# Kernel tuning notes

Measured on AMD Instinct MI355X. Metric: run time of the kernel, lower is better.

## Reference

```python
import jax, jax.numpy as jnp
import numpy as np

D = 1024

def setup_inputs() -> dict:
    key = jax.random.key(0)
    kx, kw = jax.random.split(key)
    x = jax.random.normal(kx, (4, 2048, D), dtype=jnp.float32)
    # nn.Linear(d, 3d, bias=False): weight [3d, d]; y = x @ W.T
    W = jax.random.normal(kw, (3 * D, D), dtype=jnp.float32) * (1.0 / np.sqrt(D))
    return {"x": x, "W": W}

def reference(x, W):
    d = x.shape[-1]
    qkv = jnp.einsum('bsd,ed->bse', x, W)  # [B,S,3d]
    q, k, v = jnp.split(qkv, 3, axis=2)
    att = jnp.einsum('bqd,bkd->bqk', q, k) * (1.0 / jnp.sqrt(jnp.asarray(d, x.dtype)))
    att = jax.nn.softmax(att, axis=-1)
    y = jnp.einsum('bqk,bkd->bqd', att, v)
    return y
```

## Files before the change

### kernel.cpp

```cpp
#include <hip/hip_runtime.h>
#include <hip/hip_bf16.h>

typedef __attribute__((ext_vector_type(8))) short short8;
typedef __attribute__((ext_vector_type(4))) float f32x4;

typedef unsigned short u16;

__device__ __forceinline__ u16 f32_to_bf16(float f) {
    unsigned int u = __float_as_uint(f);
    u += 0x7fffu + ((u >> 16) & 1u);
    return (u16)(u >> 16);
}
__device__ __forceinline__ float bf16_to_f32(u16 h) {
    return __uint_as_float(((unsigned int)h) << 16);
}

__device__ __forceinline__ void gload16(const u16* g, u16* lds_base) {
    __builtin_amdgcn_global_load_lds(
        (const __attribute__((address_space(1))) void*)g,
        (__attribute__((address_space(3))) void*)lds_base, 16, 0, 0);
}

__global__ void cast_inputs(const float* __restrict__ x, u16* __restrict__ Xb,
                            const float* __restrict__ W, u16* __restrict__ Wb,
                            int nx4, int nw4) {
    int i = blockIdx.x * blockDim.x + threadIdx.x;
    const float* in; u16* out; int idx;
    if (i < nx4) { in = x; out = Xb; idx = i; }
    else { idx = i - nx4; if (idx >= nw4) return; in = W; out = Wb; }
    float4 v = ((const float4*)in)[idx];
    ushort4 o;
    o.x = f32_to_bf16(v.x); o.y = f32_to_bf16(v.y);
    o.z = f32_to_bf16(v.z); o.w = f32_to_bf16(v.w);
    ((ushort4*)out)[idx] = o;
}


struct Frag128 { f32x4 acc[4][4]; int lane, wm, wn; };

__device__ __forceinline__ void gemm_core_128(
    const u16* __restrict__ A, const u16* __restrict__ Bt, int K, int lda, int ldb,
    int row0, int col0, u16* sA, u16* sB, Frag128& fr)
{
    const int t    = threadIdx.x;
    const int lane = t & 63;
    const int wave = t >> 6;
    fr.lane = lane;
    fr.wm = (wave >> 1) * 64;
    fr.wn = (wave & 1) * 64;
    const int lr = lane & 15;

#pragma unroll
    for (int i = 0; i < 4; ++i)
#pragma unroll
        for (int j = 0; j < 4; ++j)
            fr.acc[i][j] = (f32x4){0.f, 0.f, 0.f, 0.f};

    const int srow = lane >> 3;
    const int gc   = (lane & 7) ^ srow;
    for (int k0 = 0; k0 < K; k0 += 64) {
        __syncthreads();
#pragma unroll
        for (int c = 0; c < 4; ++c) {
            const int rb = c * 32 + wave * 8;
            const int r  = rb + srow;
            gload16(A  + (long long)(row0 + r) * lda + k0 + gc * 8, &sA[rb * 64]);
            gload16(Bt + (long long)(col0 + r) * ldb + k0 + gc * 8, &sB[rb * 64]);
        }
        __syncthreads();

#pragma unroll
        for (int kk = 0; kk < 64; kk += 32) {
            const int cb = (lane >> 4) + (kk >> 3);
            const int sl = (cb ^ (lr & 7)) * 8;
            short8 af[4], bf[4];
#pragma unroll
            for (int i = 0; i < 4; ++i) {
                af[i] = *(const short8*)(&sA[(fr.wm + i * 16 + lr) * 64 + sl]);
                bf[i] = *(const short8*)(&sB[(fr.wn + i * 16 + lr) * 64 + sl]);
            }
#pragma unroll
            for (int i = 0; i < 4; ++i)
#pragma unroll
                for (int j = 0; j < 4; ++j)
                    fr.acc[i][j] = __builtin_amdgcn_mfma_f32_16x16x32_bf16(
                        af[i], bf[j], fr.acc[i][j], 0, 0, 0);
        }
    }
}

struct FragN64 { f32x4 acc[2][4]; int lane, wm; };

__device__ __forceinline__ void gemm_core_n64(
    const u16* __restrict__ A, const u16* __restrict__ Bt, int K, int lda, int ldb,
    int row0, int col0, u16* sA, u16* sB, FragN64& fr)
{
    const int t    = threadIdx.x;
    const int lane = t & 63;
    const int wave = t >> 6;
    fr.lane = lane;
    fr.wm = wave * 32;
    const int lr = lane & 15;

#pragma unroll
    for (int i = 0; i < 2; ++i)
#pragma unroll
        for (int j = 0; j < 4; ++j)
            fr.acc[i][j] = (f32x4){0.f, 0.f, 0.f, 0.f};

    const int srow = lane >> 3;
    const int gc   = (lane & 7) ^ srow;
    for (int k0 = 0; k0 < K; k0 += 64) {
        __syncthreads();
#pragma unroll
        for (int c = 0; c < 4; ++c) {
            const int rb = c * 32 + wave * 8;
            gload16(A + (long long)(row0 + rb + srow) * lda + k0 + gc * 8,
                    &sA[rb * 64]);
        }
#pragma unroll
        for (int c = 0; c < 2; ++c) {
            const int rb = c * 32 + wave * 8;
            gload16(Bt + (long long)(col0 + rb + srow) * ldb + k0 + gc * 8,
                    &sB[rb * 64]);
        }
        __syncthreads();

#pragma unroll
        for (int kk = 0; kk < 64; kk += 32) {
            const int cb = (lane >> 4) + (kk >> 3);
            const int sl = (cb ^ (lr & 7)) * 8;
            short8 af[2], bf[4];
#pragma unroll
            for (int i = 0; i < 2; ++i)
                af[i] = *(const short8*)(&sA[(fr.wm + i * 16 + lr) * 64 + sl]);
#pragma unroll
            for (int j = 0; j < 4; ++j)
                bf[j] = *(const short8*)(&sB[(j * 16 + lr) * 64 + sl]);
#pragma unroll
            for (int i = 0; i < 2; ++i)
#pragma unroll
                for (int j = 0; j < 4; ++j)
                    fr.acc[i][j] = __builtin_amdgcn_mfma_f32_16x16x32_bf16(
                        af[i], bf[j], fr.acc[i][j], 0, 0, 0);
        }
    }
}


__global__ __launch_bounds__(256) void gemm_qk(
    const u16* __restrict__ Xb, const u16* __restrict__ Wb, u16* __restrict__ QK)
{
    __shared__ u16 sA[128 * 64];
    __shared__ u16 sB[128 * 64];
    const int row0 = blockIdx.y * 128;
    const int col0 = blockIdx.x * 128;
    Frag128 fr;
    gemm_core_128(Xb, Wb, 1024, 1024, 1024, row0, col0, sA, sB, fr);

    const int cr = (fr.lane >> 4) * 4;
    const int cc = fr.lane & 15;
#pragma unroll
    for (int i = 0; i < 4; ++i)
#pragma unroll
        for (int j = 0; j < 4; ++j)
#pragma unroll
            for (int r = 0; r < 4; ++r) {
                int grow = row0 + fr.wm + i * 16 + cr + r;
                int gcol = col0 + fr.wn + j * 16 + cc;
                QK[(long long)grow * 2048 + gcol] = f32_to_bf16(fr.acc[i][j][r]);
            }
}

__global__ __launch_bounds__(256) void gemm_v(
    const u16* __restrict__ Xb, const u16* __restrict__ Wv, u16* __restrict__ VT)
{
    __shared__ u16 sA[128 * 64];
    __shared__ u16 sB[64 * 64];
    const int row0 = blockIdx.y * 128;
    const int col0 = blockIdx.x * 64;
    FragN64 fr;
    gemm_core_n64(Xb, Wv, 1024, 1024, 1024, row0, col0, sA, sB, fr);

    const int cr = (fr.lane >> 4) * 4;
    const int cc = fr.lane & 15;
#pragma unroll
    for (int i = 0; i < 2; ++i) {
        int grow = row0 + fr.wm + i * 16 + cr;
        int b = grow >> 11, s = grow & 2047;
#pragma unroll
        for (int j = 0; j < 4; ++j) {
            int d = col0 + j * 16 + cc;
            ushort4 o;
            o.x = f32_to_bf16(fr.acc[i][j][0]);
            o.y = f32_to_bf16(fr.acc[i][j][1]);
            o.z = f32_to_bf16(fr.acc[i][j][2]);
            o.w = f32_to_bf16(fr.acc[i][j][3]);
            *(ushort4*)(&VT[((long long)(b * 1024 + d)) * 2048 + s]) = o;
        }
    }
}

__global__ __launch_bounds__(256) void gemm_s(
    const u16* __restrict__ QK, u16* __restrict__ S)
{
    __shared__ u16 sA[128 * 64];
    __shared__ u16 sB[128 * 64];
    const long long boff = (long long)blockIdx.z * 2048 * 2048;
    const u16* Q  = QK + boff;
    const u16* Kp = QK + boff + 1024;
    u16* Sb = S + boff;
    const int row0 = blockIdx.y * 128;
    const int col0 = blockIdx.x * 128;
    Frag128 fr;
    gemm_core_128(Q, Kp, 1024, 2048, 2048, row0, col0, sA, sB, fr);

    const int cr = (fr.lane >> 4) * 4;
    const int cc = fr.lane & 15;
#pragma unroll
    for (int i = 0; i < 4; ++i)
#pragma unroll
        for (int j = 0; j < 4; ++j)
#pragma unroll
            for (int r = 0; r < 4; ++r) {
                int grow = row0 + fr.wm + i * 16 + cr + r;
                int gcol = col0 + fr.wn + j * 16 + cc;
                Sb[(long long)grow * 2048 + gcol] = f32_to_bf16(fr.acc[i][j][r]);
            }
}

__global__ __launch_bounds__(256) void gemm_pv(
    const u16* __restrict__ P, const u16* __restrict__ VT, float* __restrict__ Y)
{
    __shared__ u16 sA[128 * 64];
    __shared__ u16 sB[64 * 64];
    const u16* Pb  = P  + (long long)blockIdx.z * 2048 * 2048;
    const u16* VTb = VT + (long long)blockIdx.z * 1024 * 2048;
    float* Yb = Y + (long long)blockIdx.z * 2048 * 1024;
    const int row0 = blockIdx.y * 128;
    const int col0 = blockIdx.x * 64;
    FragN64 fr;
    gemm_core_n64(Pb, VTb, 2048, 2048, 2048, row0, col0, sA, sB, fr);

    const int cr = (fr.lane >> 4) * 4;
    const int cc = fr.lane & 15;
#pragma unroll
    for (int i = 0; i < 2; ++i)
#pragma unroll
        for (int j = 0; j < 4; ++j)
#pragma unroll
            for (int r = 0; r < 4; ++r) {
                int grow = row0 + fr.wm + i * 16 + cr + r;
                int gcol = col0 + j * 16 + cc;
                Yb[(long long)grow * 1024 + gcol] = fr.acc[i][j][r];
            }
}

__global__ __launch_bounds__(256) void softmax_rows(
    const u16* __restrict__ S, u16* __restrict__ P, float scale)
{
    const long long row = blockIdx.x;
    const u16* s = S + row * 2048;
    u16* p = P + row * 2048;
    const int t = threadIdx.x;
    const int lane = t & 63, w = t >> 6;

    short8 raw = *(const short8*)(s + t * 8);
    float v[8];
    float m = -1e30f;
#pragma unroll
    for (int i = 0; i < 8; ++i) {
        v[i] = bf16_to_f32((u16)raw[i]) * scale;
        m = fmaxf(m, v[i]);
    }
#pragma unroll
    for (int off = 32; off > 0; off >>= 1) m = fmaxf(m, __shfl_xor(m, off, 64));
    __shared__ float sm[4], ss[4];
    if (lane == 0) sm[w] = m;
    __syncthreads();
    m = fmaxf(fmaxf(sm[0], sm[1]), fmaxf(sm[2], sm[3]));

    float sum = 0.f;
#pragma unroll
    for (int i = 0; i < 8; ++i) {
        v[i] = __expf(v[i] - m);
        sum += v[i];
    }
#pragma unroll
    for (int off = 32; off > 0; off >>= 1) sum += __shfl_xor(sum, off, 64);
    if (lane == 0) ss[w] = sum;
    __syncthreads();
    const float inv = 1.0f / (ss[0] + ss[1] + ss[2] + ss[3]);
    short8 o;
#pragma unroll
    for (int i = 0; i < 8; ++i) o[i] = (short)f32_to_bf16(v[i] * inv);
    *(short8*)(p + t * 8) = o;
}

extern "C" void kernel_launch(void* const* d_in, const int* in_sizes, int n_in,
                              void* d_out, int out_size, void* d_ws, size_t ws_size,
                              hipStream_t stream) {
    const float* x = (const float*)d_in[0];
    const float* W = (const float*)d_in[1];
    float* out = (float*)d_out;

    char* ws = (char*)d_ws;
    u16* Xb = (u16*)(ws);
    u16* Wb = (u16*)(ws + 16777216LL);
    u16* QK = (u16*)(ws + 23068672LL);
    u16* VT = (u16*)(ws + 56623104LL);
    u16* P  = (u16*)(ws + 73400320LL);
    u16* S  = (u16*)(ws + 106954752LL);

    cast_inputs<<<11264, 256, 0, stream>>>(x, Xb, W, Wb,
                                           8192 * 1024 / 4, 3072 * 1024 / 4);

    gemm_qk<<<dim3(16, 64, 1), 256, 0, stream>>>(Xb, Wb, QK);
    gemm_v<<<dim3(16, 64, 1), 256, 0, stream>>>(Xb, Wb + 2048 * 1024, VT);

    gemm_s<<<dim3(16, 16, 4), 256, 0, stream>>>(QK, S);
    softmax_rows<<<8192, 256, 0, stream>>>(S, P, 0.03125f);

    gemm_pv<<<dim3(16, 16, 4), 256, 0, stream>>>(P, VT, out);
}
```

Baseline: 273.9 us.

## Fuse all attention stages into one cooperative persistent kernel with grid syncs

```diff
diff --git a/kernel.cpp b/kernel.cpp
--- a/kernel.cpp
+++ b/kernel.cpp
@@ -1,5 +1,8 @@
 #include <hip/hip_runtime.h>
 #include <hip/hip_bf16.h>
+#include <hip/hip_cooperative_groups.h>
+
+namespace cg = cooperative_groups;
 
 typedef __attribute__((ext_vector_type(8))) short short8;
 typedef __attribute__((ext_vector_type(4))) float f32x4;
@@ -19,6 +22,278 @@
     __builtin_amdgcn_global_load_lds(
         (const __attribute__((address_space(1))) void*)g,
         (__attribute__((address_space(3))) void*)lds_base, 16, 0, 0);
+}
+
+
+struct Frag128 { f32x4 acc[4][4]; int lane, wm, wn; };
+
+__device__ __forceinline__ void gemm_core_128(
+    const u16* __restrict__ A, const u16* __restrict__ Bt, int K, int lda, int ldb,
+    int row0, int col0, u16* sA, u16* sB, Frag128& fr)
+{
+    const int t    = threadIdx.x;
+    const int lane = t & 63;
+    const int wave = t >> 6;
+    fr.lane = lane;
+    fr.wm = (wave >> 1) * 64;
+    fr.wn = (wave & 1) * 64;
+    const int lr = lane & 15;
+
+#pragma unroll
+    for (int i = 0; i < 4; ++i)
+#pragma unroll
+        for (int j = 0; j < 4; ++j)
+            fr.acc[i][j] = (f32x4){0.f, 0.f, 0.f, 0.f};
+
+    const int srow = lane >> 3;
+    const int gc   = (lane & 7) ^ srow;
+    for (int k0 = 0; k0 < K; k0 += 64) {
+        __syncthreads();
+#pragma unroll
+        for (int c = 0; c < 4; ++c) {
+            const int rb = c * 32 + wave * 8;
+            const int r  = rb + srow;
+            gload16(A  + (long long)(row0 + r) * lda + k0 + gc * 8, &sA[rb * 64]);
+            gload16(Bt + (long long)(col0 + r) * ldb + k0 + gc * 8, &sB[rb * 64]);
+        }
+        __syncthreads();
+
+#pragma unroll
+        for (int kk = 0; kk < 64; kk += 32) {
+            const int cb = (lane >> 4) + (kk >> 3);
+            const int sl = (cb ^ (lr & 7)) * 8;
+            short8 af[4], bf[4];
+#pragma unroll
+            for (int i = 0; i < 4; ++i) {
+                af[i] = *(const short8*)(&sA[(fr.wm + i * 16 + lr) * 64 + sl]);
+                bf[i] = *(const short8*)(&sB[(fr.wn + i * 16 + lr) * 64 + sl]);
+            }
+#pragma unroll
+            for (int i = 0; i < 4; ++i)
+#pragma unroll
+                for (int j = 0; j < 4; ++j)
+                    fr.acc[i][j] = __builtin_amdgcn_mfma_f32_16x16x32_bf16(
+                        af[i], bf[j], fr.acc[i][j], 0, 0, 0);
+        }
+    }
+}
+
+struct FragN64 { f32x4 acc[2][4]; int lane, wm; };
+
+__device__ __forceinline__ void gemm_core_n64(
+    const u16* __restrict__ A, const u16* __restrict__ Bt, int K, int lda, int ldb,
+    int row0, int col0, u16* sA, u16* sB, FragN64& fr)
+{
+    const int t    = threadIdx.x;
+    const int lane = t & 63;
+    const int wave = t >> 6;
+    fr.lane = lane;
+    fr.wm = wave * 32;
+    const int lr = lane & 15;
+
+#pragma unroll
+    for (int i = 0; i < 2; ++i)
+#pragma unroll
+        for (int j = 0; j < 4; ++j)
+            fr.acc[i][j] = (f32x4){0.f, 0.f, 0.f, 0.f};
+
+    const int srow = lane >> 3;
+    const int gc   = (lane & 7) ^ srow;
+    for (int k0 = 0; k0 < K; k0 += 64) {
+        __syncthreads();
+#pragma unroll
+        for (int c = 0; c < 4; ++c) {
+            const int rb = c * 32 + wave * 8;
+            gload16(A + (long long)(row0 + rb + srow) * lda + k0 + gc * 8,
+                    &sA[rb * 64]);
+        }
+#pragma unroll
+        for (int c = 0; c < 2; ++c) {
+            const int rb = c * 32 + wave * 8;
+            gload16(Bt + (long long)(col0 + rb + srow) * ldb + k0 + gc * 8,
+                    &sB[rb * 64]);
+        }
+        __syncthreads();
+
+#pragma unroll
+        for (int kk = 0; kk < 64; kk += 32) {
+            const int cb = (lane >> 4) + (kk >> 3);
+            const int sl = (cb ^ (lr & 7)) * 8;
+            short8 af[2], bf[4];
+#pragma unroll
+            for (int i = 0; i < 2; ++i)
+                af[i] = *(const short8*)(&sA[(fr.wm + i * 16 + lr) * 64 + sl]);
+#pragma unroll
+            for (int j = 0; j < 4; ++j)
+                bf[j] = *(const short8*)(&sB[(j * 16 + lr) * 64 + sl]);
+#pragma unroll
+            for (int i = 0; i < 2; ++i)
+#pragma unroll
+                for (int j = 0; j < 4; ++j)
+                    fr.acc[i][j] = __builtin_amdgcn_mfma_f32_16x16x32_bf16(
+                        af[i], bf[j], fr.acc[i][j], 0, 0, 0);
+        }
+    }
+}
+
+
+__global__ __launch_bounds__(256, 4) void attn_mega(
+    const float* __restrict__ x, const float* __restrict__ W,
+    float* __restrict__ out,
+    u16* __restrict__ Xb, u16* __restrict__ Wb, u16* __restrict__ QK,
+    u16* __restrict__ VT, u16* __restrict__ P, u16* __restrict__ S)
+{
+    __shared__ __align__(16) u16 smem[2 * 128 * 64];
+    u16* sA = smem;
+    u16* sB = smem + 128 * 64;
+
+    const int bid = blockIdx.x;
+    const int t   = threadIdx.x;
+    cg::grid_group grid = cg::this_grid();
+
+    {
+        const int NX4 = 8192 * 1024 / 4;
+        int base = bid * 256 + t;
+#pragma unroll
+        for (int it = 0; it < 11; ++it) {
+            int i = base + it * 262144;
+            const float4* src; ushort4* dst; int idx;
+            if (i < NX4) { src = (const float4*)x; dst = (ushort4*)Xb; idx = i; }
+            else { src = (const float4*)W; dst = (ushort4*)Wb; idx = i - NX4; }
+            float4 v = src[idx];
+            ushort4 o;
+            o.x = f32_to_bf16(v.x); o.y = f32_to_bf16(v.y);
+            o.z = f32_to_bf16(v.z); o.w = f32_to_bf16(v.w);
+            dst[idx] = o;
+        }
+    }
+    grid.sync();
+
+    {
+        const int row0 = (bid >> 4) * 128, col0 = (bid & 15) * 128;
+        Frag128 fr;
+        gemm_core_128(Xb, Wb, 1024, 1024, 1024, row0, col0, sA, sB, fr);
+        const int cr = (fr.lane >> 4) * 4, cc = fr.lane & 15;
+#pragma unroll
+        for (int i = 0; i < 4; ++i)
+#pragma unroll
+            for (int j = 0; j < 4; ++j)
+#pragma unroll
+                for (int r = 0; r < 4; ++r) {
+                    int grow = row0 + fr.wm + i * 16 + cr + r;
+                    int gcol = col0 + fr.wn + j * 16 + cc;
+                    QK[(long long)grow * 2048 + gcol] = f32_to_bf16(fr.acc[i][j][r]);
+                }
+    }
+
+    {
+        const int row0 = (bid >> 4) * 128, col0 = (bid & 15) * 64;
+        FragN64 fr;
+        gemm_core_n64(Xb, Wb + 2048 * 1024, 1024, 1024, 1024, row0, col0, sA, sB, fr);
+        const int cr = (fr.lane >> 4) * 4, cc = fr.lane & 15;
+#pragma unroll
+        for (int i = 0; i < 2; ++i) {
+            int grow = row0 + fr.wm + i * 16 + cr;
+            int b = grow >> 11, s = grow & 2047;
+#pragma unroll
+            for (int j = 0; j < 4; ++j) {
+                int d = col0 + j * 16 + cc;
+                ushort4 o;
+                o.x = f32_to_bf16(fr.acc[i][j][0]);
+                o.y = f32_to_bf16(fr.acc[i][j][1]);
+                o.z = f32_to_bf16(fr.acc[i][j][2]);
+                o.w = f32_to_bf16(fr.acc[i][j][3]);
+                *(ushort4*)(&VT[((long long)(b * 1024 + d)) * 2048 + s]) = o;
+            }
+        }
+    }
+    grid.sync();
+
+    {
+        const int xx = bid & 15, yy = (bid >> 4) & 15, zz = bid >> 8;
+        const long long boff = (long long)zz * 2048 * 2048;
+        const u16* Q  = QK + boff;
+        const u16* Kp = QK + boff + 1024;
+        u16* Sb = S + boff;
+        const int row0 = yy * 128, col0 = xx * 128;
+        Frag128 fr;
+        gemm_core_128(Q, Kp, 1024, 2048, 2048, row0, col0, sA, sB, fr);
+        const int cr = (fr.lane >> 4) * 4, cc = fr.lane & 15;
+#pragma unroll
+        for (int i = 0; i < 4; ++i)
+#pragma unroll
+            for (int j = 0; j < 4; ++j)
+#pragma unroll
+                for (int r = 0; r < 4; ++r) {
+                    int grow = row0 + fr.wm + i * 16 + cr + r;
+                    int gcol = col0 + fr.wn + j * 16 + cc;
+                    Sb[(long long)grow * 2048 + gcol] = f32_to_bf16(fr.acc[i][j][r]);
+                }
+    }
+    grid.sync();
+
+    {
+        float* red = (float*)smem;
+        const int lane = t & 63, w = t >> 6;
+#pragma unroll 1
+        for (int r8 = 0; r8 < 8; ++r8) {
+            const long long row = (long long)bid * 8 + r8;
+            const u16* s = S + row * 2048;
+            u16* p = P + row * 2048;
+            short8 raw = *(const short8*)(s + t * 8);
+            float v[8];
+            float m = -1e30f;
+#pragma unroll
+            for (int i = 0; i < 8; ++i) {
+                v[i] = bf16_to_f32((u16)raw[i]) * 0.03125f;
+                m = fmaxf(m, v[i]);
+            }
+#pragma unroll
+            for (int off = 32; off > 0; off >>= 1) m = fmaxf(m, __shfl_xor(m, off, 64));
+            __syncthreads();
+            if (lane == 0) red[w] = m;
+            __syncthreads();
+            m = fmaxf(fmaxf(red[0], red[1]), fmaxf(red[2], red[3]));
+            float sum = 0.f;
+#pragma unroll
+            for (int i = 0; i < 8; ++i) {
+                v[i] = __expf(v[i] - m);
+                sum += v[i];
+            }
+#pragma unroll
+            for (int off = 32; off > 0; off >>= 1) sum += __shfl_xor(sum, off, 64);
+            __syncthreads();
+            if (lane == 0) red[4 + w] = sum;
+            __syncthreads();
+            const float inv = 1.0f / (red[4] + red[5] + red[6] + red[7]);
+            short8 o;
+#pragma unroll
+            for (int i = 0; i < 8; ++i) o[i] = (short)f32_to_bf16(v[i] * inv);
+            *(short8*)(p + t * 8) = o;
+        }
+    }
+    grid.sync();
+
+    {
+        const int xx = bid & 15, yy = (bid >> 4) & 15, zz = bid >> 8;
+        const u16* Pb  = P  + (long long)zz * 2048 * 2048;
+        const u16* VTb = VT + (long long)zz * 1024 * 2048;
+        float* Yb = out + (long long)zz * 2048 * 1024;
+        const int row0 = yy * 128, col0 = xx * 64;
+        FragN64 fr;
+        gemm_core_n64(Pb, VTb, 2048, 2048, 2048, row0, col0, sA, sB, fr);
+        const int cr = (fr.lane >> 4) * 4, cc = fr.lane & 15;
+#pragma unroll
+        for (int i = 0; i < 2; ++i)
+#pragma unroll
+            for (int j = 0; j < 4; ++j)
+#pragma unroll
+                for (int r = 0; r < 4; ++r) {
+                    int grow = row0 + fr.wm + i * 16 + cr + r;
+                    int gcol = col0 + j * 16 + cc;
+                    Yb[(long long)grow * 1024 + gcol] = fr.acc[i][j][r];
+                }
+    }
 }
 
 __global__ void cast_inputs(const float* __restrict__ x, u16* __restrict__ Xb,
@@ -35,119 +310,6 @@
     ((ushort4*)out)[idx] = o;
 }
 
-
-struct Frag128 { f32x4 acc[4][4]; int lane, wm, wn; };
-
-__device__ __forceinline__ void gemm_core_128(
-    const u16* __restrict__ A, const u16* __restrict__ Bt, int K, int lda, int ldb,
-    int row0, int col0, u16* sA, u16* sB, Frag128& fr)
-{
-    const int t    = threadIdx.x;
-    const int lane = t & 63;
-    const int wave = t >> 6;
-    fr.lane = lane;
-    fr.wm = (wave >> 1) * 64;
-    fr.wn = (wave & 1) * 64;
-    const int lr = lane & 15;
-
-#pragma unroll
-    for (int i = 0; i < 4; ++i)
-#pragma unroll
-        for (int j = 0; j < 4; ++j)
-            fr.acc[i][j] = (f32x4){0.f, 0.f, 0.f, 0.f};
-
-    const int srow = lane >> 3;
-    const int gc   = (lane & 7) ^ srow;
-    for (int k0 = 0; k0 < K; k0 += 64) {
-        __syncthreads();
-#pragma unroll
-        for (int c = 0; c < 4; ++c) {
-            const int rb = c * 32 + wave * 8;
-            const int r  = rb + srow;
-            gload16(A  + (long long)(row0 + r) * lda + k0 + gc * 8, &sA[rb * 64]);
-            gload16(Bt + (long long)(col0 + r) * ldb + k0 + gc * 8, &sB[rb * 64]);
-        }
-        __syncthreads();
-
-#pragma unroll
-        for (int kk = 0; kk < 64; kk += 32) {
-            const int cb = (lane >> 4) + (kk >> 3);
-            const int sl = (cb ^ (lr & 7)) * 8;
-            short8 af[4], bf[4];
-#pragma unroll
-            for (int i = 0; i < 4; ++i) {
-                af[i] = *(const short8*)(&sA[(fr.wm + i * 16 + lr) * 64 + sl]);
-                bf[i] = *(const short8*)(&sB[(fr.wn + i * 16 + lr) * 64 + sl]);
-            }
-#pragma unroll
-            for (int i = 0; i < 4; ++i)
-#pragma unroll
-                for (int j = 0; j < 4; ++j)
-                    fr.acc[i][j] = __builtin_amdgcn_mfma_f32_16x16x32_bf16(
-                        af[i], bf[j], fr.acc[i][j], 0, 0, 0);
-        }
-    }
-}
-
-struct FragN64 { f32x4 acc[2][4]; int lane, wm; };
-
-__device__ __forceinline__ void gemm_core_n64(
-    const u16* __restrict__ A, const u16* __restrict__ Bt, int K, int lda, int ldb,
-    int row0, int col0, u16* sA, u16* sB, FragN64& fr)
-{
-    const int t    = threadIdx.x;
-    const int lane = t & 63;
-    const int wave = t >> 6;
-    fr.lane = lane;
-    fr.wm = wave * 32;
-    const int lr = lane & 15;
-
-#pragma unroll
-    for (int i = 0; i < 2; ++i)
-#pragma unroll
-        for (int j = 0; j < 4; ++j)
-            fr.acc[i][j] = (f32x4){0.f, 0.f, 0.f, 0.f};
-
-    const int srow = lane >> 3;
-    const int gc   = (lane & 7) ^ srow;
-    for (int k0 = 0; k0 < K; k0 += 64) {
-        __syncthreads();
-#pragma unroll
-        for (int c = 0; c < 4; ++c) {
-            const int rb = c * 32 + wave * 8;
-            gload16(A + (long long)(row0 + rb + srow) * lda + k0 + gc * 8,
-                    &sA[rb * 64]);
-        }
-#pragma unroll
-        for (int c = 0; c < 2; ++c) {
-            const int rb = c * 32 + wave * 8;
-            gload16(Bt + (long long)(col0 + rb + srow) * ldb + k0 + gc * 8,
-                    &sB[rb * 64]);
-        }
-        __syncthreads();
-
-#pragma unroll
-        for (int kk = 0; kk < 64; kk += 32) {
-            const int cb = (lane >> 4) + (kk >> 3);
-            const int sl = (cb ^ (lr & 7)) * 8;
-            short8 af[2], bf[4];
-#pragma unroll
-            for (int i = 0; i < 2; ++i)
-                af[i] = *(const short8*)(&sA[(fr.wm + i * 16 + lr) * 64 + sl]);
-#pragma unroll
-            for (int j = 0; j < 4; ++j)
-                bf[j] = *(const short8*)(&sB[(j * 16 + lr) * 64 + sl]);
-#pragma unroll
-            for (int i = 0; i < 2; ++i)
-#pragma unroll
-                for (int j = 0; j < 4; ++j)
-                    fr.acc[i][j] = __builtin_amdgcn_mfma_f32_16x16x32_bf16(
-                        af[i], bf[j], fr.acc[i][j], 0, 0, 0);
-        }
-    }
-}
-
-
 __global__ __launch_bounds__(256) void gemm_qk(
     const u16* __restrict__ Xb, const u16* __restrict__ Wb, u16* __restrict__ QK)
 {
@@ -157,9 +319,7 @@
     const int col0 = blockIdx.x * 128;
     Frag128 fr;
     gemm_core_128(Xb, Wb, 1024, 1024, 1024, row0, col0, sA, sB, fr);
-
-    const int cr = (fr.lane >> 4) * 4;
-    const int cc = fr.lane & 15;
+    const int cr = (fr.lane >> 4) * 4, cc = fr.lane & 15;
 #pragma unroll
     for (int i = 0; i < 4; ++i)
 #pragma unroll
@@ -181,9 +341,7 @@
     const int col0 = blockIdx.x * 64;
     FragN64 fr;
     gemm_core_n64(Xb, Wv, 1024, 1024, 1024, row0, col0, sA, sB, fr);
-
-    const int cr = (fr.lane >> 4) * 4;
-    const int cc = fr.lane & 15;
+    const int cr = (fr.lane >> 4) * 4, cc = fr.lane & 15;
 #pragma unroll
     for (int i = 0; i < 2; ++i) {
         int grow = row0 + fr.wm + i * 16 + cr;
@@ -214,9 +372,7 @@
     const int col0 = blockIdx.x * 128;
     Frag128 fr;
     gemm_core_128(Q, Kp, 1024, 2048, 2048, row0, col0, sA, sB, fr);
-
-    const int cr = (fr.lane >> 4) * 4;
-    const int cc = fr.lane & 15;
+    const int cr = (fr.lane >> 4) * 4, cc = fr.lane & 15;
 #pragma unroll
     for (int i = 0; i < 4; ++i)
 #pragma unroll
@@ -241,9 +397,7 @@
     const int col0 = blockIdx.x * 64;
     FragN64 fr;
     gemm_core_n64(Pb, VTb, 2048, 2048, 2048, row0, col0, sA, sB, fr);
-
-    const int cr = (fr.lane >> 4) * 4;
-    const int cc = fr.lane & 15;
+    const int cr = (fr.lane >> 4) * 4, cc = fr.lane & 15;
 #pragma unroll
     for (int i = 0; i < 2; ++i)
 #pragma unroll
@@ -264,7 +418,6 @@
     u16* p = P + row * 2048;
     const int t = threadIdx.x;
     const int lane = t & 63, w = t >> 6;
-
     short8 raw = *(const short8*)(s + t * 8);
     float v[8];
     float m = -1e30f;
@@ -279,7 +432,6 @@
     if (lane == 0) sm[w] = m;
     __syncthreads();
     m = fmaxf(fmaxf(sm[0], sm[1]), fmaxf(sm[2], sm[3]));
-
     float sum = 0.f;
 #pragma unroll
     for (int i = 0; i < 8; ++i) {
@@ -312,14 +464,24 @@
     u16* P  = (u16*)(ws + 73400320LL);
     u16* S  = (u16*)(ws + 106954752LL);
 
-    cast_inputs<<<11264, 256, 0, stream>>>(x, Xb, W, Wb,
-                                           8192 * 1024 / 4, 3072 * 1024 / 4);
-
-    gemm_qk<<<dim3(16, 64, 1), 256, 0, stream>>>(Xb, Wb, QK);
-    gemm_v<<<dim3(16, 64, 1), 256, 0, stream>>>(Xb, Wb + 2048 * 1024, VT);
-
-    gemm_s<<<dim3(16, 16, 4), 256, 0, stream>>>(QK, S);
-    softmax_rows<<<8192, 256, 0, stream>>>(S, P, 0.03125f);
-
-    gemm_pv<<<dim3(16, 16, 4), 256, 0, stream>>>(P, VT, out);
-}
+    int maxb = 0;
+    hipError_t oe = hipOccupancyMaxActiveBlocksPerMultiprocessor(
+        &maxb, attn_mega, 256, 0);
+    const bool coop = (oe == hipSuccess && maxb >= 4);
+
+    if (coop) {
+        void* args[] = {(void*)&x, (void*)&W, (void*)&out,
+                        (void*)&Xb, (void*)&Wb, (void*)&QK,
+                        (void*)&VT, (void*)&P, (void*)&S};
+        hipLaunchCooperativeKernel(attn_mega, dim3(1024), dim3(256), args, 0,
+                                   stream);
+    } else {
+        cast_inputs<<<11264, 256, 0, stream>>>(x, Xb, W, Wb,
+                                               8192 * 1024 / 4, 3072 * 1024 / 4);
+        gemm_qk<<<dim3(16, 64, 1), 256, 0, stream>>>(Xb, Wb, QK);
+        gemm_v<<<dim3(16, 64, 1), 256, 0, stream>>>(Xb, Wb + 2048 * 1024, VT);
+        gemm_s<<<dim3(16, 16, 4), 256, 0, stream>>>(QK, S);
+        softmax_rows<<<8192, 256, 0, stream>>>(S, P, 0.03125f);
+        gemm_pv<<<dim3(16, 16, 4), 256, 0, stream>>>(P, VT, out);
+    }
+}
```

After: 277.1 us. Within noise of the previous version (+1.2%).
